# Kernel tuning notes

Hardware: AMD Instinct MI355X
Metric: run time of the kernel (lower is better)

The kernel has to match this reference:

```python
import jax, jax.numpy as jnp
import numpy as np

L, T, F, DIM = 16, 16384, 2, 3
N_MIN, N_MAX = 16.0, 512.0
N_PTS = 262144
# torch code builds np.int32 primes [1, 2654435761, 805459861]; 2654435761 wraps to -1640531535.
# Since T is a power of two, int32 wraparound multiply/xor followed by nonnegative mod T gives
# bit-identical indices to the int64 torch computation.
PIS = jnp.array([1, -1640531535, 805459861], dtype=jnp.int32)
# corner ordering from get_indices: corner k = a*4+b*2+c with a->dim0, b->dim1, c->dim2
OFFS = jnp.array([[(k >> 2) & 1, (k >> 1) & 1, k & 1] for k in range(8)], dtype=jnp.float32)  # (8,3)


def setup_inputs() -> dict:
    key = jax.random.key(0)
    k1, k2 = jax.random.split(key)
    x = jax.random.uniform(k1, (N_PTS, DIM), dtype=jnp.float32)
    # nn.init.uniform_(weight, a=-1e-4, b=1e-4) for each of L tables of shape (T, F)
    embeddings = jax.random.uniform(k2, (L, T, F), minval=-1e-4, maxval=1e-4, dtype=jnp.float32)
    return {"x": x, "embeddings": embeddings}


def reference(x, embeddings):
    # per-level growth factor b = exp((log Nmax - log Nmin)/L); N_l = Nmin * b**l
    b = jnp.exp((jnp.log(N_MAX) - jnp.log(N_MIN)) / L)
    N_l = N_MIN * b ** jnp.arange(L, dtype=jnp.float32)                      # (L,)
    un_x = x[None, :, :] * N_l[:, None, None]                                # (L,N,3)  (mu=0, sigma=1)
    lo = jnp.floor(un_x)
    hi = jnp.ceil(un_x)
    d = hi - lo                                                              # (L,N,3)
    nz = d != 0
    diff = jnp.where(nz, (un_x - lo) / jnp.where(nz, d, 1.0), 0.0)           # (L,N,3)

    mask = OFFS.astype(bool)[None, None]                                     # (1,1,8,3)
    corners = jnp.where(mask, hi[:, :, None, :], lo[:, :, None, :])          # (L,N,8,3)
    ci = corners.astype(jnp.int32)
    prod = ci * PIS                                                          # (L,N,8,3) wrapping int32 mul
    idx = jnp.mod(prod[..., 0] ^ prod[..., 1] ^ prod[..., 2], T)             # (L,N,8)

    # per-level table gather: (L,T,F)[ (L,N,8) ] -> (L,N,8,F)
    feats = jax.vmap(lambda emb, i: emb[i])(embeddings, idx)

    # trilinear weights: prod over dims of (diff if corner bit else 1-diff)
    w = jnp.prod(jnp.where(mask, diff[:, :, None, :], 1.0 - diff[:, :, None, :]), axis=-1)  # (L,N,8)
    c = jnp.einsum('lnc,lncf->lnf', w, feats)                                # (L,N,F)
    return jnp.transpose(c, (1, 0, 2)).reshape(x.shape[0], L * F)            # (N, L*F)
```

## Files before the change

kernel.cpp:

```cpp
#include <hip/hip_runtime.h>
#include <stdint.h>

constexpr int L_LEVELS = 16;
constexpr int T_SIZE   = 16384;
constexpr int N_PTS    = 262144;

typedef _Float16 h2 __attribute__((ext_vector_type(2)));
typedef _Float16 h4 __attribute__((ext_vector_type(4)));
typedef _Float16 h8 __attribute__((ext_vector_type(8)));

constexpr uint32_t P1_4 = 2654435761u * 4u;
constexpr uint32_t P2_4 = 805459861u * 4u;
constexpr uint32_t M4   = (T_SIZE - 1) * 4u;

__device__ __forceinline__ h2 lerp2(h2 a, h2 b, h2 t) {
    return a + t * (b - a);
}


__global__ __launch_bounds__(256) void cvt_tables(
    const float* __restrict__ emb, h2* __restrict__ tbl)
{
    const int i = blockIdx.x * 256 + threadIdx.x;
    const float4* __restrict__ s = reinterpret_cast<const float4*>(emb);
    float4 a = s[2 * i];
    float4 b = s[2 * i + 1];
    h8 w = { (_Float16)a.x, (_Float16)a.y, (_Float16)a.z, (_Float16)a.w,
             (_Float16)b.x, (_Float16)b.y, (_Float16)b.z, (_Float16)b.w };
    reinterpret_cast<h8*>(tbl)[i] = w;
}

__global__ __launch_bounds__(512, 2) void hash_encode_groups(
    const float* __restrict__ x,
    const h2*    __restrict__ tbl,
    h2*          __restrict__ res)
{
    __shared__ h2 tab[2][T_SIZE];

    const int t     = threadIdx.x;
    const int chunk = blockIdx.x & 63;
    const int L0    = (blockIdx.x >> 6) * 4;
    const int n0    = chunk * 4096 + t * 8;

    {
        const h8* __restrict__ s =
            reinterpret_cast<const h8*>(tbl + (size_t)L0 * T_SIZE);
        h8* __restrict__ d = reinterpret_cast<h8*>(tab[0]);
#pragma unroll
        for (int r = 0; r < 8; ++r) {
            const int j = r * 512 + t;
            d[j] = s[j];
        }
    }

    union { float4 q[6]; float f[24]; } xs;
    {
        const float4* __restrict__ xv =
            reinterpret_cast<const float4*>(x + (size_t)n0 * 3);
#pragma unroll
        for (int i = 0; i < 6; ++i) xs.q[i] = xv[i];
    }
    __syncthreads();

#pragma unroll
    for (int l = 0; l < 4; ++l) {
        h8 stg[8];
        if (l < 3) {
            const h8* __restrict__ s = reinterpret_cast<const h8*>(
                tbl + (size_t)(L0 + l + 1) * T_SIZE);
#pragma unroll
            for (int r = 0; r < 8; ++r) stg[r] = s[r * 512 + t];
        }

        const float Nl = 16.0f * exp2f((float)(L0 + l) * 0.3125f);
        const char* __restrict__ tb =
            reinterpret_cast<const char*>(tab[l & 1]);

        union { h2 r[8]; float4 q[2]; } out8;

#pragma unroll
        for (int p = 0; p < 8; ++p) {
            const float u0 = xs.f[3 * p + 0] * Nl;
            const float u1 = xs.f[3 * p + 1] * Nl;
            const float u2 = xs.f[3 * p + 2] * Nl;

            const float fl0 = floorf(u0), fl1 = floorf(u1), fl2 = floorf(u2);
            const float df0 = u0 - fl0, df1 = u1 - fl1, df2 = u2 - fl2;

            const uint32_t q0 = ((uint32_t)(int32_t)fl0) << 2;
            const uint32_t q1 = ((uint32_t)(int32_t)fl1) * P1_4;
            const uint32_t q2 = ((uint32_t)(int32_t)fl2) * P2_4;
            const uint32_t d0 = (q0 ^ (q0 + 4u))   & M4;
            const uint32_t d1 = (q1 ^ (q1 + P1_4)) & M4;
            const uint32_t d2 = (q2 ^ (q2 + P2_4)) & M4;

            uint32_t off = (q0 ^ q1 ^ q2) & M4;

            constexpr int gray[8] = {0, 1, 3, 2, 6, 7, 5, 4};
            h2 f[8];
#pragma unroll
            for (int j = 0; j < 8; ++j) {
                f[gray[j]] = *reinterpret_cast<const h2*>(tb + off);
                if (j < 7) {
                    const int tog = gray[j] ^ gray[j + 1];
                    off ^= (tog == 4) ? d0 : (tog == 2) ? d1 : d2;
                }
            }

            const _Float16 h0 = (_Float16)df0, h1 = (_Float16)df1,
                           hv2 = (_Float16)df2;
            const h2 t0 = {h0, h0}, t1 = {h1, h1}, t2 = {hv2, hv2};
            h2 e0 = lerp2(f[0], f[1], t2);
            h2 e1 = lerp2(f[2], f[3], t2);
            h2 e2 = lerp2(f[4], f[5], t2);
            h2 e3 = lerp2(f[6], f[7], t2);
            h2 g0 = lerp2(e0, e1, t1);
            h2 g1 = lerp2(e2, e3, t1);
            out8.r[p] = lerp2(g0, g1, t0);
        }

        {
            float4* __restrict__ o4 = reinterpret_cast<float4*>(
                res + (size_t)(L0 + l) * N_PTS + n0);
            o4[0] = out8.q[0];
            o4[1] = out8.q[1];
        }

        if (l < 3) {
            h8* __restrict__ d = reinterpret_cast<h8*>(tab[(l + 1) & 1]);
#pragma unroll
            for (int r = 0; r < 8; ++r) d[r * 512 + t] = stg[r];
            __syncthreads();
        }
    }
}

__global__ __launch_bounds__(256) void transpose_expand(
    const h2* __restrict__ res,
    float4*   __restrict__ out)
{
    __shared__ h2 tile[L_LEVELS][514];
    const int t    = threadIdx.x;
    const int base = blockIdx.x * 512;

#pragma unroll
    for (int l = 0; l < L_LEVELS; ++l) {
        h4 v = reinterpret_cast<const h4*>(res + (size_t)l * N_PTS + base)[t];
        *reinterpret_cast<h4*>(&tile[l][2 * t]) = v;
    }
    __syncthreads();

    float4* __restrict__ o = out + (size_t)base * 8;
#pragma unroll
    for (int i = 0; i < L_LEVELS; ++i) {
        const int f    = i * 256 + t;
        const int p    = f >> 3;
        const int part = f & 7;
        h2 a = tile[2 * part][p];
        h2 b = tile[2 * part + 1][p];
        o[f] = make_float4((float)a.x, (float)a.y,
                           (float)b.x, (float)b.y);
    }
}

__global__ __launch_bounds__(1024, 4) void hash_encode_fused(
    const float* __restrict__ x,
    const float* __restrict__ emb,
    float4*      __restrict__ out)
{
    __shared__ union {
        h2 tab[2][T_SIZE];
        h2 tr[1024][20];
    } sm;

    const int t = threadIdx.x;
    const int n = blockIdx.x * 1024 + t;
    const int rot = (blockIdx.x << 4) & 4095;

    const float x0 = x[3 * n + 0];
    const float x1 = x[3 * n + 1];
    const float x2 = x[3 * n + 2];

    {
        const float4* __restrict__ s = reinterpret_cast<const float4*>(emb);
        h8* __restrict__ d = reinterpret_cast<h8*>(sm.tab[0]);
#pragma unroll
        for (int r = 0; r < 4; ++r) {
            const int j = (r * 1024 + t + rot) & 4095;
            float4 a = s[2 * j];
            float4 b = s[2 * j + 1];
            h8 w = { (_Float16)a.x, (_Float16)a.y, (_Float16)a.z, (_Float16)a.w,
                     (_Float16)b.x, (_Float16)b.y, (_Float16)b.z, (_Float16)b.w };
            d[j] = w;
        }
    }
    __syncthreads();

    union { h2 r[L_LEVELS]; h8 q[4]; } resu;

#pragma unroll
    for (int l = 0; l < L_LEVELS; ++l) {
        float4 sa0, sb0, sa1, sb1, sa2, sb2, sa3, sb3;
        int j0 = 0, j1 = 0, j2 = 0, j3 = 0;
        if (l < L_LEVELS - 1) {
            const float4* __restrict__ s = reinterpret_cast<const float4*>(
                emb + (size_t)(l + 1) * T_SIZE * 2);
            j0 = (0 * 1024 + t + rot) & 4095;
            j1 = (1 * 1024 + t + rot) & 4095;
            j2 = (2 * 1024 + t + rot) & 4095;
            j3 = (3 * 1024 + t + rot) & 4095;
            sa0 = s[2 * j0]; sb0 = s[2 * j0 + 1];
            sa1 = s[2 * j1]; sb1 = s[2 * j1 + 1];
            sa2 = s[2 * j2]; sb2 = s[2 * j2 + 1];
            sa3 = s[2 * j3]; sb3 = s[2 * j3 + 1];
        }

        const float Nl = 16.0f * exp2f((float)l * 0.3125f);
        const char* __restrict__ tb =
            reinterpret_cast<const char*>(sm.tab[l & 1]);

        const float u0 = x0 * Nl, u1 = x1 * Nl, u2 = x2 * Nl;
        const float fl0 = floorf(u0), fl1 = floorf(u1), fl2 = floorf(u2);
        const float df0 = u0 - fl0, df1 = u1 - fl1, df2 = u2 - fl2;

        const uint32_t q0 = ((uint32_t)(int32_t)fl0) << 2;
        const uint32_t q1 = ((uint32_t)(int32_t)fl1) * P1_4;
        const uint32_t q2 = ((uint32_t)(int32_t)fl2) * P2_4;
        const uint32_t d0 = (q0 ^ (q0 + 4u))   & M4;
        const uint32_t d1 = (q1 ^ (q1 + P1_4)) & M4;
        const uint32_t d2 = (q2 ^ (q2 + P2_4)) & M4;

        uint32_t off = (q0 ^ q1 ^ q2) & M4;

        constexpr int gray[8] = {0, 1, 3, 2, 6, 7, 5, 4};
        h2 f[8];
#pragma unroll
        for (int j = 0; j < 8; ++j) {
            f[gray[j]] = *reinterpret_cast<const h2*>(tb + off);
            if (j < 7) {
                const int tog = gray[j] ^ gray[j + 1];
                off ^= (tog == 4) ? d0 : (tog == 2) ? d1 : d2;
            }
        }

        const _Float16 h0 = (_Float16)df0, h1 = (_Float16)df1, hv2 = (_Float16)df2;
        const h2 t0 = {h0, h0}, t1 = {h1, h1}, t2 = {hv2, hv2};
        h2 e0 = lerp2(f[0], f[1], t2);
        h2 e1 = lerp2(f[2], f[3], t2);
        h2 e2 = lerp2(f[4], f[5], t2);
        h2 e3 = lerp2(f[6], f[7], t2);
        h2 g0 = lerp2(e0, e1, t1);
        h2 g1 = lerp2(e2, e3, t1);
        resu.r[l] = lerp2(g0, g1, t0);

        if (l < L_LEVELS - 1) {
            h8* __restrict__ d = reinterpret_cast<h8*>(sm.tab[(l + 1) & 1]);
            h8 w0 = { (_Float16)sa0.x, (_Float16)sa0.y, (_Float16)sa0.z, (_Float16)sa0.w,
                      (_Float16)sb0.x, (_Float16)sb0.y, (_Float16)sb0.z, (_Float16)sb0.w };
            h8 w1 = { (_Float16)sa1.x, (_Float16)sa1.y, (_Float16)sa1.z, (_Float16)sa1.w,
                      (_Float16)sb1.x, (_Float16)sb1.y, (_Float16)sb1.z, (_Float16)sb1.w };
            h8 w2 = { (_Float16)sa2.x, (_Float16)sa2.y, (_Float16)sa2.z, (_Float16)sa2.w,
                      (_Float16)sb2.x, (_Float16)sb2.y, (_Float16)sb2.z, (_Float16)sb2.w };
            h8 w3 = { (_Float16)sa3.x, (_Float16)sa3.y, (_Float16)sa3.z, (_Float16)sa3.w,
                      (_Float16)sb3.x, (_Float16)sb3.y, (_Float16)sb3.z, (_Float16)sb3.w };
            d[j0] = w0;
            d[j1] = w1;
            d[j2] = w2;
            d[j3] = w3;
            __syncthreads();
        }
    }

    __syncthreads();
#pragma unroll
    for (int g = 0; g < 4; ++g)
        *reinterpret_cast<h8*>(&sm.tr[t][4 * g]) = resu.q[g];
    __syncthreads();

    float4* __restrict__ o = out + (size_t)blockIdx.x * 8192;
#pragma unroll
    for (int i = 0; i < 8; ++i) {
        const int p  = i * 128 + (t >> 3);
        const int l0 = 2 * (t & 7);
        h4 v = *reinterpret_cast<const h4*>(&sm.tr[p][l0]);
        o[i * 1024 + t] = make_float4((float)v.x, (float)v.y,
                                      (float)v.z, (float)v.w);
    }
}

extern "C" void kernel_launch(void* const* d_in, const int* in_sizes, int n_in,
                              void* d_out, int out_size, void* d_ws, size_t ws_size,
                              hipStream_t stream) {
    const float* x   = (const float*)d_in[0];
    const float* emb = (const float*)d_in[1];

    const size_t RES_OFF = (size_t)2 << 20;
    const size_t need    = RES_OFF + (size_t)L_LEVELS * N_PTS * sizeof(h2);

    if (ws_size >= need) {
        h2* tbl = (h2*)d_ws;
        h2* res = (h2*)((char*)d_ws + RES_OFF);
        cvt_tables<<<256, 256, 0, stream>>>(emb, tbl);
        hash_encode_groups<<<256, 512, 0, stream>>>(x, tbl, res);
        transpose_expand<<<512, 256, 0, stream>>>(res, (float4*)d_out);
    } else {
        hash_encode_fused<<<256, 1024, 0, stream>>>(x, emb, (float4*)d_out);
    }
}
```

Measured before the change: 89.69 us.

## Split hash-encode work into one block per level and chunk

```diff
diff --git a/kernel.cpp b/kernel.cpp
--- a/kernel.cpp
+++ b/kernel.cpp
@@ -30,22 +30,22 @@
     reinterpret_cast<h8*>(tbl)[i] = w;
 }
 
-__global__ __launch_bounds__(512, 2) void hash_encode_groups(
+__global__ __launch_bounds__(512, 4) void hash_encode_level(
     const float* __restrict__ x,
     const h2*    __restrict__ tbl,
     h2*          __restrict__ res)
 {
-    __shared__ h2 tab[2][T_SIZE];
+    __shared__ h2 tab[T_SIZE];
 
     const int t     = threadIdx.x;
-    const int chunk = blockIdx.x & 63;
-    const int L0    = (blockIdx.x >> 6) * 4;
+    const int l     = blockIdx.x & (L_LEVELS - 1);
+    const int chunk = blockIdx.x >> 4;
     const int n0    = chunk * 4096 + t * 8;
 
     {
         const h8* __restrict__ s =
-            reinterpret_cast<const h8*>(tbl + (size_t)L0 * T_SIZE);
-        h8* __restrict__ d = reinterpret_cast<h8*>(tab[0]);
+            reinterpret_cast<const h8*>(tbl + (size_t)l * T_SIZE);
+        h8* __restrict__ d = reinterpret_cast<h8*>(tab);
 #pragma unroll
         for (int r = 0; r < 8; ++r) {
             const int j = r * 512 + t;
@@ -62,76 +62,57 @@
     }
     __syncthreads();
 
-#pragma unroll
-    for (int l = 0; l < 4; ++l) {
-        h8 stg[8];
-        if (l < 3) {
-            const h8* __restrict__ s = reinterpret_cast<const h8*>(
-                tbl + (size_t)(L0 + l + 1) * T_SIZE);
-#pragma unroll
-            for (int r = 0; r < 8; ++r) stg[r] = s[r * 512 + t];
-        }
-
-        const float Nl = 16.0f * exp2f((float)(L0 + l) * 0.3125f);
-        const char* __restrict__ tb =
-            reinterpret_cast<const char*>(tab[l & 1]);
-
-        union { h2 r[8]; float4 q[2]; } out8;
-
-#pragma unroll
-        for (int p = 0; p < 8; ++p) {
-            const float u0 = xs.f[3 * p + 0] * Nl;
-            const float u1 = xs.f[3 * p + 1] * Nl;
-            const float u2 = xs.f[3 * p + 2] * Nl;
-
-            const float fl0 = floorf(u0), fl1 = floorf(u1), fl2 = floorf(u2);
-            const float df0 = u0 - fl0, df1 = u1 - fl1, df2 = u2 - fl2;
-
-            const uint32_t q0 = ((uint32_t)(int32_t)fl0) << 2;
-            const uint32_t q1 = ((uint32_t)(int32_t)fl1) * P1_4;
-            const uint32_t q2 = ((uint32_t)(int32_t)fl2) * P2_4;
-            const uint32_t d0 = (q0 ^ (q0 + 4u))   & M4;
-            const uint32_t d1 = (q1 ^ (q1 + P1_4)) & M4;
-            const uint32_t d2 = (q2 ^ (q2 + P2_4)) & M4;
-
-            uint32_t off = (q0 ^ q1 ^ q2) & M4;
-
-            constexpr int gray[8] = {0, 1, 3, 2, 6, 7, 5, 4};
-            h2 f[8];
-#pragma unroll
-            for (int j = 0; j < 8; ++j) {
-                f[gray[j]] = *reinterpret_cast<const h2*>(tb + off);
-                if (j < 7) {
-                    const int tog = gray[j] ^ gray[j + 1];
-                    off ^= (tog == 4) ? d0 : (tog == 2) ? d1 : d2;
-                }
+    const float Nl = 16.0f * exp2f((float)l * 0.3125f);
+    const char* __restrict__ tb = reinterpret_cast<const char*>(tab);
+
+    union { h2 r[8]; float4 q[2]; } out8;
+
+#pragma unroll
+    for (int p = 0; p < 8; ++p) {
+        const float u0 = xs.f[3 * p + 0] * Nl;
+        const float u1 = xs.f[3 * p + 1] * Nl;
+        const float u2 = xs.f[3 * p + 2] * Nl;
+
+        const float fl0 = floorf(u0), fl1 = floorf(u1), fl2 = floorf(u2);
+        const float df0 = u0 - fl0, df1 = u1 - fl1, df2 = u2 - fl2;
+
+        const uint32_t q0 = ((uint32_t)(int32_t)fl0) << 2;
+        const uint32_t q1 = ((uint32_t)(int32_t)fl1) * P1_4;
+        const uint32_t q2 = ((uint32_t)(int32_t)fl2) * P2_4;
+        const uint32_t d0 = (q0 ^ (q0 + 4u))   & M4;
+        const uint32_t d1 = (q1 ^ (q1 + P1_4)) & M4;
+        const uint32_t d2 = (q2 ^ (q2 + P2_4)) & M4;
+
+        uint32_t off = (q0 ^ q1 ^ q2) & M4;
+
+        constexpr int gray[8] = {0, 1, 3, 2, 6, 7, 5, 4};
+        h2 f[8];
+#pragma unroll
+        for (int j = 0; j < 8; ++j) {
+            f[gray[j]] = *reinterpret_cast<const h2*>(tb + off);
+            if (j < 7) {
+                const int tog = gray[j] ^ gray[j + 1];
+                off ^= (tog == 4) ? d0 : (tog == 2) ? d1 : d2;
             }
-
-            const _Float16 h0 = (_Float16)df0, h1 = (_Float16)df1,
-                           hv2 = (_Float16)df2;
-            const h2 t0 = {h0, h0}, t1 = {h1, h1}, t2 = {hv2, hv2};
-            h2 e0 = lerp2(f[0], f[1], t2);
-            h2 e1 = lerp2(f[2], f[3], t2);
-            h2 e2 = lerp2(f[4], f[5], t2);
-            h2 e3 = lerp2(f[6], f[7], t2);
-            h2 g0 = lerp2(e0, e1, t1);
-            h2 g1 = lerp2(e2, e3, t1);
-            out8.r[p] = lerp2(g0, g1, t0);
-        }
-
-        {
-            float4* __restrict__ o4 = reinterpret_cast<float4*>(
-                res + (size_t)(L0 + l) * N_PTS + n0);
-            o4[0] = out8.q[0];
-            o4[1] = out8.q[1];
-        }
-
-        if (l < 3) {
-            h8* __restrict__ d = reinterpret_cast<h8*>(tab[(l + 1) & 1]);
-#pragma unroll
-            for (int r = 0; r < 8; ++r) d[r * 512 + t] = stg[r];
-            __syncthreads();
-        }
+        }
+
+        const _Float16 h0 = (_Float16)df0, h1 = (_Float16)df1,
+                       hv2 = (_Float16)df2;
+        const h2 t0 = {h0, h0}, t1 = {h1, h1}, t2 = {hv2, hv2};
+        h2 e0 = lerp2(f[0], f[1], t2);
+        h2 e1 = lerp2(f[2], f[3], t2);
+        h2 e2 = lerp2(f[4], f[5], t2);
+        h2 e3 = lerp2(f[6], f[7], t2);
+        h2 g0 = lerp2(e0, e1, t1);
+        h2 g1 = lerp2(e2, e3, t1);
+        out8.r[p] = lerp2(g0, g1, t0);
+    }
+
+    {
+        float4* __restrict__ o4 = reinterpret_cast<float4*>(
+            res + (size_t)l * N_PTS + n0);
+        o4[0] = out8.q[0];
+        o4[1] = out8.q[1];
     }
 }
 
@@ -301,7 +282,7 @@
         h2* tbl = (h2*)d_ws;
         h2* res = (h2*)((char*)d_ws + RES_OFF);
         cvt_tables<<<256, 256, 0, stream>>>(emb, tbl);
-        hash_encode_groups<<<256, 512, 0, stream>>>(x, tbl, res);
+        hash_encode_level<<<1024, 512, 0, stream>>>(x, tbl, res);
         transpose_expand<<<512, 256, 0, stream>>>(res, (float4*)d_out);
     } else {
         hash_encode_fused<<<256, 1024, 0, stream>>>(x, emb, (float4*)d_out);
```

Measured after the change: 87.38 us. 1.03x faster.
